# Kernel tuning notes

Measured on AMD Instinct MI355X. Metric: run time of the kernel, lower is better.

The kernel has to match this reference:

```python
import jax, jax.numpy as jnp
import numpy as np

B, N, D, H, A = 1024, 16, 64, 64, 64
TAU = 0.01   # gumbel-softmax temperature from the source
EPS = 1e-10


def setup_inputs() -> dict:
    key = jax.random.key(0)
    ks = jax.random.split(key, 23)

    def rn(k, shape, s=0.05):
        return jax.random.normal(k, shape, dtype=jnp.float32) * s

    return {
        "obs": jax.random.normal(ks[0], (B, N, D), dtype=jnp.float32),
        "hidden_state": jax.random.normal(ks[1], (B * N, A), dtype=jnp.float32),
        "gumbel_u": jax.random.uniform(ks[2], (B * N * (N - 1), 2), dtype=jnp.float32,
                                       minval=1e-6, maxval=1.0 - 1e-6),
        "W_enc": rn(ks[3], (D, H)), "b_enc": rn(ks[4], (H,)),
        "Wih_f": rn(ks[5], (3 * H, 2 * H)), "Whh_f": rn(ks[6], (3 * H, H)),
        "bih_f": rn(ks[7], (3 * H,)), "bhh_f": rn(ks[8], (3 * H,)),
        "Wih_b": rn(ks[9], (3 * H, 2 * H)), "Whh_b": rn(ks[10], (3 * H, H)),
        "bih_b": rn(ks[11], (3 * H,)), "bhh_b": rn(ks[12], (3 * H,)),
        "W_hard": rn(ks[13], (2 * H, 2)), "b_hard": rn(ks[14], (2,)),
        "Wq": rn(ks[15], (H, A)), "Wk": rn(ks[16], (H, A)),
        "Wv": rn(ks[17], (H, A)), "b_v": rn(ks[18], (A,)),
        "Wih_c": rn(ks[19], (3 * A, A)), "Whh_c": rn(ks[20], (3 * A, A)),
        "bih_c": rn(ks[21], (3 * A,)), "bhh_c": rn(ks[22], (3 * A,)),
    }


def _gru_scan(x_seq, Wih, Whh, bih, bhh):
    # x_seq: [T, BN, 2H]; PyTorch GRU gate order r, z, n. Input projection
    # for all timesteps is precomputed (one big GEMM) outside the scan.
    gi = jnp.einsum('tbd,gd->tbg', x_seq, Wih) + bih  # [T, BN, 3H]
    h0 = jnp.zeros((x_seq.shape[1], Whh.shape[1]), x_seq.dtype)

    def step(h, gi_t):
        gh = h @ Whh.T + bhh
        i_r, i_z, i_n = jnp.split(gi_t, 3, axis=-1)
        h_r, h_z, h_n = jnp.split(gh, 3, axis=-1)
        r = jax.nn.sigmoid(i_r + h_r)
        z = jax.nn.sigmoid(i_z + h_z)
        n = jnp.tanh(i_n + r * h_n)
        h_new = (1.0 - z) * n + z * h
        return h_new, h_new

    _, out = jax.lax.scan(step, h0, gi)
    return out  # [T, BN, H]


def _gru_cell(x, h, Wih, Whh, bih, bhh):
    gi = x @ Wih.T + bih
    gh = h @ Whh.T + bhh
    i_r, i_z, i_n = jnp.split(gi, 3, axis=-1)
    h_r, h_z, h_n = jnp.split(gh, 3, axis=-1)
    r = jax.nn.sigmoid(i_r + h_r)
    z = jax.nn.sigmoid(i_z + h_z)
    n = jnp.tanh(i_n + r * h_n)
    return (1.0 - z) * n + z * h


def reference(obs, hidden_state, gumbel_u, W_enc, b_enc,
              Wih_f, Whh_f, bih_f, bhh_f, Wih_b, Whh_b, bih_b, bhh_b,
              W_hard, b_hard, Wq, Wk, Wv, b_v,
              Wih_c, Whh_c, bih_c, bhh_c):
    b, n, d = obs.shape
    h_enc = jax.nn.relu(obs @ W_enc + b_enc)          # [B, N, H]
    h_flat = h_enc.reshape(-1, H)                      # [B*N, H]

    # static neighbor index table: row i lists all j != i
    j_idx = np.array([[j for j in range(n) if j != i] for i in range(n)])  # [N, N-1]

    # pairwise concat features, vectorized (replaces the double python loop)
    h_j = h_enc[:, j_idx]                               # [B, N, N-1, H]
    h_i = jnp.broadcast_to(h_enc[:, :, None, :], h_j.shape)
    pair = jnp.concatenate([h_i, h_j], axis=-1)        # [B, N, N-1, 2H]
    input_hard = pair.transpose(2, 0, 1, 3).reshape(n - 1, b * n, 2 * H)

    # bidirectional GRU over the N-1 neighbor axis
    out_f = _gru_scan(input_hard, Wih_f, Whh_f, bih_f, bhh_f)
    out_b = _gru_scan(input_hard[::-1], Wih_b, Whh_b, bih_b, bhh_b)[::-1]
    h_hard = jnp.concatenate([out_f, out_b], axis=-1)  # [N-1, B*N, 2H]
    h_hard = h_hard.transpose(1, 0, 2).reshape(-1, 2 * H)

    # hard gate: gumbel-softmax (soft sample, tau=0.01), take channel 1
    logits = h_hard @ W_hard + b_hard                   # [B*N*(N-1), 2]
    g = -jnp.log(-jnp.log(gumbel_u + EPS) + EPS)
    hard = jax.nn.softmax((logits + g) / TAU, axis=-1)
    hard_w = hard[:, 1].reshape(b, n, n - 1)            # [B, N, N-1]

    # scaled dot-product attention over neighbors j != i
    q = (h_flat @ Wq).reshape(b, n, A)
    k = (h_flat @ Wk).reshape(b, n, A)
    v = jax.nn.relu(h_flat @ Wv + b_v).reshape(b, n, A)
    k_j = k[:, j_idx]                                   # [B, N, N-1, A]
    v_j = v[:, j_idx]
    score = jnp.einsum('bna,bnja->bnj', q, k_j) / float(np.sqrt(A))
    soft = jax.nn.softmax(score, axis=-1)
    x = jnp.einsum('bnja,bnj->bna', v_j, soft * hard_w).reshape(b * n, A)

    return _gru_cell(x, hidden_state, Wih_c, Whh_c, bih_c, bhh_c)
```

## Files before the change

kernel.cpp:

```cpp
#include <hip/hip_runtime.h>
#include <hip/hip_bf16.h>
#include <stdint.h>

#define NNODE 16384
#define TAU_ 0.01f
#define EPSG 1e-10f

#define OFF_WENC 0
#define OFF_BENC 4096
#define OFF_WIHF_H 4160
#define OFF_WIHF_L 16448
#define OFF_WHHF_H 28736
#define OFF_BIHF 41024
#define OFF_BHHF 41216
#define OFF_WIHB_H 41408
#define OFF_WIHB_L 53696
#define OFF_WHHB_H 65984
#define OFF_BIHB 78272
#define OFF_BHHB 78464
#define OFF_WHARD 78656
#define OFF_BHARD 78912
#define OFF_WQT_H 78914
#define OFF_WQT_L 80962
#define OFF_WKT_H 83010
#define OFF_WKT_L 85058
#define OFF_WVT_H 87106
#define OFF_WVT_L 89154
#define OFF_BV 91202
#define OFF_WIHC_H 91266
#define OFF_WIHC_L 97410
#define OFF_WHHC_H 103554
#define OFF_WHHC_L 109698
#define OFF_BIHC 115842
#define OFF_BHHC 116034
#define OFF_WENCT_H 118784
#define OFF_WENCT_L 120832
#define OFF_YF 131072
#define OFF_YB (OFF_YF + 491520)
#define WS_FLOATS (OFF_YB + 491520)

typedef float  v4f __attribute__((ext_vector_type(4)));
typedef short  v8s __attribute__((ext_vector_type(8)));

__device__ __forceinline__ float rcpf(float x){ return __builtin_amdgcn_rcpf(x); }
__device__ __forceinline__ float sigf(float x){ return rcpf(1.0f + __expf(-x)); }
__device__ __forceinline__ float tanhfast(float x){ return 1.0f - 2.0f*rcpf(__expf(2.0f*x)+1.0f); }
__device__ __forceinline__ unsigned short f2bf(float f){
  __hip_bfloat16 h = __float2bfloat16(f);
  return *reinterpret_cast<unsigned short*>(&h);
}
__device__ __forceinline__ float bf2f(unsigned short u){
  union { unsigned int i; float f; } v; v.i = ((unsigned int)u) << 16; return v.f;
}

struct Prep {
  const float* s[20];
  int n[20];
  int o[20];
};
__global__ void k_prep(Prep p, float* __restrict__ ws){
  int a = blockIdx.y;
  int i = blockIdx.x * blockDim.x + threadIdx.x;
  if (i < p.n[a]) ws[p.o[a] + i] = p.s[a][i];
}

__global__ void k_prep2(const float* __restrict__ wenc,
                        const float* __restrict__ wihf, const float* __restrict__ wihb,
                        const float* __restrict__ whhf, const float* __restrict__ whhb,
                        const float* __restrict__ wq,   const float* __restrict__ wk,
                        const float* __restrict__ wv,   const float* __restrict__ wihc,
                        const float* __restrict__ whhc,
                        float* __restrict__ ws){
  int a = blockIdx.y;
  int i = blockIdx.x * blockDim.x + threadIdx.x;
  if (a == 0 || (a >= 5 && a <= 7)){
    if (i < 4096){
      const float* src = (a==0) ? wenc : (a==5) ? wq : (a==6) ? wk : wv;
      int oh = (a==0) ? OFF_WENCT_H : (a==5) ? OFF_WQT_H : (a==6) ? OFF_WKT_H : OFF_WVT_H;
      int ol = (a==0) ? OFF_WENCT_L : oh + 2048;
      float x = src[((i & 63) << 6) | (i >> 6)];
      unsigned short h = f2bf(x);
      unsigned short l = f2bf(x - bf2f(h));
      ((unsigned short*)(ws + oh))[i] = h;
      ((unsigned short*)(ws + ol))[i] = l;
    }
  } else if (a == 1 || a == 2){
    if (i < 24576){
      float x = (a == 1 ? wihf : wihb)[i];
      unsigned short h = f2bf(x);
      unsigned short l = f2bf(x - bf2f(h));
      ((unsigned short*)(ws + (a == 1 ? OFF_WIHF_H : OFF_WIHB_H)))[i] = h;
      ((unsigned short*)(ws + (a == 1 ? OFF_WIHF_L : OFF_WIHB_L)))[i] = l;
    }
  } else if (a == 3 || a == 4){
    if (i < 12288){
      float x = (a == 3 ? whhf : whhb)[i];
      ((unsigned short*)(ws + (a == 3 ? OFF_WHHF_H : OFF_WHHB_H)))[i] = f2bf(x);
    }
  } else {
    if (i < 12288){
      float x = (a == 8 ? wihc : whhc)[i];
      unsigned short h = f2bf(x);
      unsigned short l = f2bf(x - bf2f(h));
      int oh = (a == 8 ? OFF_WIHC_H : OFF_WHHC_H);
      ((unsigned short*)(ws + oh))[i] = h;
      ((unsigned short*)(ws + oh + 6144))[i] = l;
    }
  }
}

__global__ __launch_bounds__(256, 2) void k_main(const float* __restrict__ obs,
                                                 const float* __restrict__ hid,
                                                 const float* __restrict__ gum,
                                                 float* __restrict__ ws,
                                                 float* __restrict__ out){
  __shared__ float smem[10176];
  float* s_u2 = smem;
  unsigned short* s_B = (unsigned short*)(smem + 6272);
  unsigned short* s_obs_h = s_B;
  unsigned short* s_obs_l = s_B + 1152;
  float* s_red = smem + 9088;
  float* s_y   = smem + 9216;
  float* s_q  = smem;
  float* s_k  = smem + 1088;
  float* s_v  = smem + 2176;
  float* s_co = smem + 3264;

  const int tid = threadIdx.x;
  const int nl  = tid & 63;
  const int grp = __builtin_amdgcn_readfirstlane(tid >> 6);
  const int dir = grp >> 1;
  const int lw  = grp & 1;
  const int hi2 = grp;
  const int q4  = nl >> 4;
  const int i_c = nl & 15;
  const int node = i_c;
  const int base = blockIdx.x * 16;

  {
    float4 a = *(const float4*)&obs[base*64 + tid*4];
    int nn = tid >> 4, d0 = (tid & 15)*4;
    unsigned short hh[4], ll[4];
    float xs[4] = {a.x,a.y,a.z,a.w};
    #pragma unroll
    for (int e = 0; e < 4; e++){
      hh[e] = f2bf(xs[e]);
      ll[e] = f2bf(xs[e] - bf2f(hh[e]));
    }
    *(uint2*)&s_obs_h[nn*72 + d0] = make_uint2((unsigned)hh[0] | ((unsigned)hh[1]<<16),
                                               (unsigned)hh[2] | ((unsigned)hh[3]<<16));
    *(uint2*)&s_obs_l[nn*72 + d0] = make_uint2((unsigned)ll[0] | ((unsigned)ll[1]<<16),
                                               (unsigned)ll[2] | ((unsigned)ll[3]<<16));
  }
  __syncthreads();

  const float* benc = ws + OFF_BENC;
  const unsigned short* wtH = (const unsigned short*)(ws + OFF_WENCT_H);
  const unsigned short* wtL = (const unsigned short*)(ws + OFF_WENCT_L);
  v4f dEnc;
  {
    v8s obH[2], obL[2];
    #pragma unroll
    for (int kc = 0; kc < 2; kc++){
      int ba = node*72 + kc*32 + q4*8;
      obH[kc] = *(const v8s*)&s_obs_h[ba];
      obL[kc] = *(const v8s*)&s_obs_l[ba];
    }
    float4 bi = *(const float4*)&benc[16*hi2 + 4*q4];
    v4f d = (v4f){bi.x, bi.y, bi.z, bi.w};
    #pragma unroll
    for (int kc = 0; kc < 2; kc++){
      int aa = (16*hi2 + i_c)*64 + kc*32 + q4*8;
      v8s aH = *(const v8s*)&wtH[aa];
      v8s aL = *(const v8s*)&wtL[aa];
      d = __builtin_amdgcn_mfma_f32_16x16x32_bf16(aH, obH[kc], d, 0,0,0);
      d = __builtin_amdgcn_mfma_f32_16x16x32_bf16(aH, obL[kc], d, 0,0,0);
      d = __builtin_amdgcn_mfma_f32_16x16x32_bf16(aL, obH[kc], d, 0,0,0);
    }
    dEnc = d;
  }
  __syncthreads();
  {
    unsigned short hh[4], ll[4];
    #pragma unroll
    for (int r = 0; r < 4; r++){
      float v = fmaxf(dEnc[r], 0.0f);
      hh[r] = f2bf(v);
      ll[r] = f2bf(v - bf2f(hh[r]));
    }
    int wa = node*72 + 16*hi2 + 4*q4;
    *(uint2*)&s_obs_h[wa] = make_uint2((unsigned)hh[0] | ((unsigned)hh[1]<<16),
                                       (unsigned)hh[2] | ((unsigned)hh[3]<<16));
    *(uint2*)&s_obs_l[wa] = make_uint2((unsigned)ll[0] | ((unsigned)ll[1]<<16),
                                       (unsigned)ll[2] | ((unsigned)ll[3]<<16));
  }
  __syncthreads();

  v8s hbH[2], hbL[2];
  #pragma unroll
  for (int kc = 0; kc < 2; kc++){
    int ba = node*72 + kc*32 + q4*8;
    hbH[kc] = *(const v8s*)&s_obs_h[ba];
    hbL[kc] = *(const v8s*)&s_obs_l[ba];
  }

  v4f dq, dk, dv;
  {
    const unsigned short* wqH = (const unsigned short*)(ws + OFF_WQT_H);
    const unsigned short* wqL = (const unsigned short*)(ws + OFF_WQT_L);
    const unsigned short* wkH = (const unsigned short*)(ws + OFF_WKT_H);
    const unsigned short* wkL = (const unsigned short*)(ws + OFF_WKT_L);
    const unsigned short* wvH = (const unsigned short*)(ws + OFF_WVT_H);
    const unsigned short* wvL = (const unsigned short*)(ws + OFF_WVT_L);
    const float* bv = ws + OFF_BV;
    v4f q_ = (v4f){0.f,0.f,0.f,0.f};
    v4f k_ = (v4f){0.f,0.f,0.f,0.f};
    float4 b4 = *(const float4*)&bv[16*hi2 + 4*q4];
    v4f v_ = (v4f){b4.x, b4.y, b4.z, b4.w};
    #pragma unroll
    for (int kc = 0; kc < 2; kc++){
      int ai = (16*hi2 + i_c)*64 + kc*32 + q4*8;
      v8s aH = *(const v8s*)&wqH[ai]; v8s aL = *(const v8s*)&wqL[ai];
      q_ = __builtin_amdgcn_mfma_f32_16x16x32_bf16(aH, hbH[kc], q_, 0,0,0);
      q_ = __builtin_amdgcn_mfma_f32_16x16x32_bf16(aH, hbL[kc], q_, 0,0,0);
      q_ = __builtin_amdgcn_mfma_f32_16x16x32_bf16(aL, hbH[kc], q_, 0,0,0);
      aH = *(const v8s*)&wkH[ai]; aL = *(const v8s*)&wkL[ai];
      k_ = __builtin_amdgcn_mfma_f32_16x16x32_bf16(aH, hbH[kc], k_, 0,0,0);
      k_ = __builtin_amdgcn_mfma_f32_16x16x32_bf16(aH, hbL[kc], k_, 0,0,0);
      k_ = __builtin_amdgcn_mfma_f32_16x16x32_bf16(aL, hbH[kc], k_, 0,0,0);
      aH = *(const v8s*)&wvH[ai]; aL = *(const v8s*)&wvL[ai];
      v_ = __builtin_amdgcn_mfma_f32_16x16x32_bf16(aH, hbH[kc], v_, 0,0,0);
      v_ = __builtin_amdgcn_mfma_f32_16x16x32_bf16(aH, hbL[kc], v_, 0,0,0);
      v_ = __builtin_amdgcn_mfma_f32_16x16x32_bf16(aL, hbH[kc], v_, 0,0,0);
    }
    dq = q_; dk = k_; dv = v_;
  }

  const float* bih = ws + (dir ? OFF_BIHB : OFF_BIHF);
  const float* bhh = ws + (dir ? OFF_BHHB : OFF_BHHF);
  const unsigned short* wiH = (const unsigned short*)(ws + (dir ? OFF_WIHB_H : OFF_WIHF_H));
  const unsigned short* wiL = (const unsigned short*)(ws + (dir ? OFF_WIHB_L : OFF_WIHF_L));
  const unsigned short* whH = (const unsigned short*)(ws + (dir ? OFF_WHHB_H : OFF_WHHF_H));
  float* myu2 = s_u2 + dir*3136;

  #pragma unroll
  for (int m = 0; m < 6; m++){
    int T = 6*lw + m;
    v4f d = (v4f){0.f,0.f,0.f,0.f};
    #pragma unroll
    for (int kc = 0; kc < 2; kc++){
      int aa = (16*T + i_c)*128 + 64 + kc*32 + q4*8;
      v8s aH = *(const v8s*)&wiH[aa];
      v8s aL = *(const v8s*)&wiL[aa];
      d = __builtin_amdgcn_mfma_f32_16x16x32_bf16(aH, hbH[kc], d, 0,0,0);
      d = __builtin_amdgcn_mfma_f32_16x16x32_bf16(aH, hbL[kc], d, 0,0,0);
      d = __builtin_amdgcn_mfma_f32_16x16x32_bf16(aL, hbH[kc], d, 0,0,0);
    }
    *(v4f*)&myu2[node*196 + 16*T + 4*q4] = d;
  }

  v4f cbr[2], cbz[2], cbn[2], bhn4[2];
  #pragma unroll
  for (int g = 0; g < 3; g++){
    #pragma unroll
    for (int t2 = 0; t2 < 2; t2++){
      int row0 = 64*g + 32*lw + 16*t2 + 4*q4;
      float4 bi = *(const float4*)&bih[row0];
      v4f d;
      if (g < 2){
        float4 bh = *(const float4*)&bhh[row0];
        d = (v4f){bi.x+bh.x, bi.y+bh.y, bi.z+bh.z, bi.w+bh.w};
      } else {
        d = (v4f){bi.x, bi.y, bi.z, bi.w};
      }
      int T = (64*g + 32*lw + 16*t2) >> 4;
      #pragma unroll
      for (int kc = 0; kc < 2; kc++){
        int aa = (16*T + i_c)*128 + kc*32 + q4*8;
        v8s aH = *(const v8s*)&wiH[aa];
        v8s aL = *(const v8s*)&wiL[aa];
        d = __builtin_amdgcn_mfma_f32_16x16x32_bf16(aH, hbH[kc], d, 0,0,0);
        d = __builtin_amdgcn_mfma_f32_16x16x32_bf16(aH, hbL[kc], d, 0,0,0);
        d = __builtin_amdgcn_mfma_f32_16x16x32_bf16(aL, hbH[kc], d, 0,0,0);
      }
      if (g == 0) cbr[t2] = d; else if (g == 1) cbz[t2] = d; else cbn[t2] = d;
    }
  }
  #pragma unroll
  for (int t2 = 0; t2 < 2; t2++){
    int row0 = 128 + 32*lw + 16*t2 + 4*q4;
    float4 nh = *(const float4*)&bhh[row0];
    bhn4[t2] = (v4f){nh.x, nh.y, nh.z, nh.w};
  }

  v8s afr[2][2], afz[2][2], afn[2][2];
  #pragma unroll
  for (int t2 = 0; t2 < 2; t2++){
    #pragma unroll
    for (int kc = 0; kc < 2; kc++){
      #pragma unroll
      for (int g = 0; g < 3; g++){
        int row = g*64 + 32*lw + 16*t2 + i_c;
        v8s a = *(const v8s*)&whH[row*64 + kc*32 + q4*8];
        if (g == 0) afr[t2][kc] = a; else if (g == 1) afz[t2][kc] = a; else afn[t2][kc] = a;
      }
    }
  }

  const float* whard = ws + OFF_WHARD + dir*128;
  float wh0[8], wh1[8];
  #pragma unroll
  for (int t2 = 0; t2 < 2; t2++){
    #pragma unroll
    for (int r = 0; r < 4; r++){
      int l = 32*lw + 16*t2 + 4*q4 + r;
      wh0[t2*4+r] = whard[l*2];
      wh1[t2*4+r] = whard[l*2+1];
    }
  }
  __syncthreads();

  unsigned short* myh = s_B + dir*2816;
  float hv[8];
  #pragma unroll
  for (int m = 0; m < 8; m++) hv[m] = 0.0f;

  for (int kk = 0; kk < 15; kk++){
    const int t  = dir ? (14 - kk) : kk;
    const int j  = t + (t >= i_c ? 1 : 0);
    const int jl = j;
    const int rb = kk & 1;
    const int wb = (kk + 1) & 1;

    v8s b0, b1;
    if (kk > 0){
      const unsigned short* rp = myh + rb*1408 + node*88 + q4*8;
      b0 = *(const v8s*)(rp);
      b1 = *(const v8s*)(rp + 32);
    }

    float a0p = 0.f, a1p = 0.f;
    #pragma unroll
    for (int t2 = 0; t2 < 2; t2++){
      int l0 = 32*lw + 16*t2 + 4*q4;
      v4f dr = cbr[t2], dz = cbz[t2];
      v4f dn = (v4f){0.f,0.f,0.f,0.f};
      if (kk > 0){
        dr = __builtin_amdgcn_mfma_f32_16x16x32_bf16(afr[t2][0], b0, dr, 0,0,0);
        dr = __builtin_amdgcn_mfma_f32_16x16x32_bf16(afr[t2][1], b1, dr, 0,0,0);
        dz = __builtin_amdgcn_mfma_f32_16x16x32_bf16(afz[t2][0], b0, dz, 0,0,0);
        dz = __builtin_amdgcn_mfma_f32_16x16x32_bf16(afz[t2][1], b1, dz, 0,0,0);
        dn = __builtin_amdgcn_mfma_f32_16x16x32_bf16(afn[t2][0], b0, dn, 0,0,0);
        dn = __builtin_amdgcn_mfma_f32_16x16x32_bf16(afn[t2][1], b1, dn, 0,0,0);
      }
      v4f ur = *(const v4f*)&myu2[jl*196 +       l0];
      v4f uz = *(const v4f*)&myu2[jl*196 +  64 + l0];
      v4f un = *(const v4f*)&myu2[jl*196 + 128 + l0];
      float hn[4];
      #pragma unroll
      for (int r = 0; r < 4; r++){
        float rg = sigf(dr[r] + ur[r]);
        float zg = sigf(dz[r] + uz[r]);
        float ng = tanhfast(cbn[t2][r] + un[r] + rg*(bhn4[t2][r] + dn[r]));
        float hnew = (1.0f - zg)*ng + zg*hv[t2*4+r];
        hv[t2*4+r] = hnew;
        hn[r] = hnew;
        a0p += hnew*wh0[t2*4+r];
        a1p += hnew*wh1[t2*4+r];
      }
      unsigned int p0 = (unsigned int)f2bf(hn[0]) | ((unsigned int)f2bf(hn[1]) << 16);
      unsigned int p1 = (unsigned int)f2bf(hn[2]) | ((unsigned int)f2bf(hn[3]) << 16);
      *(uint2*)(myh + wb*1408 + node*88 + l0) = make_uint2(p0, p1);
    }

    a0p += __shfl_xor(a0p, 16); a0p += __shfl_xor(a0p, 32);
    a1p += __shfl_xor(a1p, 16); a1p += __shfl_xor(a1p, 32);
    float* sr = s_red + dir*64 + rb*32;
    if (lw == 0 && q4 == 0)
      *(float2*)&sr[node*2] = make_float2(a0p, a1p);
    __syncthreads();
    if (lw == 1 && q4 == 0){
      float2 pp = *(const float2*)&sr[node*2];
      *(float2*)&s_y[dir*480 + (node*15 + t)*2] = make_float2(a0p + pp.x, a1p + pp.y);
    }
  }
  __syncthreads();

  {
    *(v4f*)&s_q[node*68 + 16*hi2 + 4*q4] = dq;
    #pragma unroll
    for (int r = 0; r < 4; r++){
      s_k[(16*hi2 + 4*q4 + r)*17 + node] = dk[r];
      s_v[(16*hi2 + 4*q4 + r)*17 + node] = fmaxf(dv[r], 0.f);
    }
  }
  __syncthreads();

  const int n2  = tid >> 3;
  const int asl = tid & 7;
  if (tid < 128){
    float4 aq0 = *(const float4*)&s_q[n2*68 + asl*8];
    float4 aq1 = *(const float4*)&s_q[n2*68 + asl*8 + 4];
    float sc[15];
    #pragma unroll
    for (int t = 0; t < 15; t++){
      int jl = t + (t >= n2 ? 1 : 0);
      const float* kp = s_k + (asl*8)*17 + jl;
      float s = aq0.x*kp[0]  + aq0.y*kp[17]  + aq0.z*kp[34]  + aq0.w*kp[51]
              + aq1.x*kp[68] + aq1.y*kp[85]  + aq1.z*kp[102] + aq1.w*kp[119];
      s += __shfl_xor(s, 1); s += __shfl_xor(s, 2); s += __shfl_xor(s, 4);
      sc[t] = s * 0.125f;
    }
    float m = sc[0];
    #pragma unroll
    for (int t = 1; t < 15; t++) m = fmaxf(m, sc[t]);
    float den = 0.f;
    #pragma unroll
    for (int t = 0; t < 15; t++) den += __expf(sc[t]-m);
    float rden = rcpf(den);
    const float bh0 = ws[OFF_BHARD], bh1 = ws[OFF_BHARD+1];
    #pragma unroll
    for (int t = 0; t < 15; t++){
      if ((t & 7) == asl){
        int yi = (n2*15 + t)*2;
        float y0 = s_y[yi]     + s_y[480 + yi]     + bh0;
        float y1 = s_y[yi + 1] + s_y[480 + yi + 1] + bh1;
        float2 u2 = *(const float2*)&gum[((base + n2)*15 + t)*2];
        float g0 = -__logf(-__logf(u2.x + EPSG) + EPSG);
        float g1 = -__logf(-__logf(u2.y + EPSG) + EPSG);
        float w  = sigf(((y1+g1) - (y0+g0)) * (1.0f/TAU_));
        s_co[t*16 + n2] = __expf(sc[t]-m)*rden*w;
      }
    }
  }
  __syncthreads();

  unsigned short* s_xh  = s_B;
  unsigned short* s_xl  = s_B + 1152;
  unsigned short* s_h0h = s_B + 2304;
  unsigned short* s_h0l = s_B + 3456;
  if (tid < 128){
    float xa[8];
    #pragma unroll
    for (int il = 0; il < 8; il++) xa[il] = 0.f;
    #pragma unroll
    for (int t = 0; t < 15; t++){
      float c = s_co[t*16 + n2];
      int jl = t + (t >= n2 ? 1 : 0);
      const float* vp = s_v + (asl*8)*17 + jl;
      xa[0] += c*vp[0];   xa[1] += c*vp[17];  xa[2] += c*vp[34];  xa[3] += c*vp[51];
      xa[4] += c*vp[68];  xa[5] += c*vp[85];  xa[6] += c*vp[102]; xa[7] += c*vp[119];
    }
    union { v8s v; unsigned short u[8]; } XH, XL;
    #pragma unroll
    for (int e = 0; e < 8; e++){
      XH.u[e] = f2bf(xa[e]);
      XL.u[e] = f2bf(xa[e] - bf2f(XH.u[e]));
    }
    *(v8s*)&s_xh[n2*72 + asl*8] = XH.v;
    *(v8s*)&s_xl[n2*72 + asl*8] = XL.v;
  }
  {
    float4 a = *(const float4*)&hid[base*64 + tid*4];
    int nn = tid >> 4, d0 = (tid & 15)*4;
    unsigned short hh[4], ll[4];
    float xs[4] = {a.x,a.y,a.z,a.w};
    #pragma unroll
    for (int e = 0; e < 4; e++){
      hh[e] = f2bf(xs[e]);
      ll[e] = f2bf(xs[e] - bf2f(hh[e]));
    }
    *(uint2*)&s_h0h[nn*72 + d0] = make_uint2((unsigned)hh[0] | ((unsigned)hh[1]<<16),
                                             (unsigned)hh[2] | ((unsigned)hh[3]<<16));
    *(uint2*)&s_h0l[nn*72 + d0] = make_uint2((unsigned)ll[0] | ((unsigned)ll[1]<<16),
                                             (unsigned)ll[2] | ((unsigned)ll[3]<<16));
  }
  __syncthreads();

  {
    v8s xbH[2], xbL[2], h0H[2], h0L[2];
    #pragma unroll
    for (int kc = 0; kc < 2; kc++){
      int ba = node*72 + kc*32 + q4*8;
      xbH[kc] = *(const v8s*)&s_xh[ba];  xbL[kc] = *(const v8s*)&s_xl[ba];
      h0H[kc] = *(const v8s*)&s_h0h[ba]; h0L[kc] = *(const v8s*)&s_h0l[ba];
    }
    const unsigned short* wiH2 = (const unsigned short*)(ws + OFF_WIHC_H);
    const unsigned short* wiL2 = (const unsigned short*)(ws + OFF_WIHC_L);
    const unsigned short* whH2 = (const unsigned short*)(ws + OFF_WHHC_H);
    const unsigned short* whL2 = (const unsigned short*)(ws + OFF_WHHC_L);
    const float* bihc = ws + OFF_BIHC; const float* bhhc = ws + OFF_BHHC;
    v4f gi[3], gh[3];
    #pragma unroll
    for (int g = 0; g < 3; g++){
      int row0 = g*64 + 16*hi2 + 4*q4;
      float4 bi = *(const float4*)&bihc[row0];
      float4 bh = *(const float4*)&bhhc[row0];
      v4f di, dh;
      if (g < 2){
        di = (v4f){bi.x+bh.x, bi.y+bh.y, bi.z+bh.z, bi.w+bh.w};
        dh = (v4f){0.f,0.f,0.f,0.f};
      } else {
        di = (v4f){bi.x, bi.y, bi.z, bi.w};
        dh = (v4f){bh.x, bh.y, bh.z, bh.w};
      }
      #pragma unroll
      for (int kc = 0; kc < 2; kc++){
        int ai = (g*64 + 16*hi2 + i_c)*64 + kc*32 + q4*8;
        v8s aH = *(const v8s*)&wiH2[ai]; v8s aL = *(const v8s*)&wiL2[ai];
        di = __builtin_amdgcn_mfma_f32_16x16x32_bf16(aH, xbH[kc], di, 0,0,0);
        di = __builtin_amdgcn_mfma_f32_16x16x32_bf16(aH, xbL[kc], di, 0,0,0);
        di = __builtin_amdgcn_mfma_f32_16x16x32_bf16(aL, xbH[kc], di, 0,0,0);
        aH = *(const v8s*)&whH2[ai]; aL = *(const v8s*)&whL2[ai];
        dh = __builtin_amdgcn_mfma_f32_16x16x32_bf16(aH, h0H[kc], dh, 0,0,0);
        dh = __builtin_amdgcn_mfma_f32_16x16x32_bf16(aH, h0L[kc], dh, 0,0,0);
        dh = __builtin_amdgcn_mfma_f32_16x16x32_bf16(aL, h0H[kc], dh, 0,0,0);
      }
      gi[g] = di; gh[g] = dh;
    }
    int l0 = 16*hi2 + 4*q4;
    float4 h04 = *(const float4*)&hid[(base+node)*64 + l0];
    float hh4[4] = {h04.x, h04.y, h04.z, h04.w};
    float ho[4];
    #pragma unroll
    for (int r = 0; r < 4; r++){
      float rg = sigf(gi[0][r] + gh[0][r]);
      float zg = sigf(gi[1][r] + gh[1][r]);
      float ng = tanhfast(gi[2][r] + rg*gh[2][r]);
      ho[r] = (1.0f - zg)*ng + zg*hh4[r];
    }
    *(float4*)&out[(base+node)*64 + l0] = make_float4(ho[0], ho[1], ho[2], ho[3]);
  }
}

extern "C" void kernel_launch(void* const* d_in, const int* in_sizes, int n_in,
                              void* d_out, int out_size, void* d_ws, size_t ws_size,
                              hipStream_t stream){
  if (ws_size < (size_t)WS_FLOATS * sizeof(float)) return;
  float* ws = (float*)d_ws;
  static const int offs[20] = {OFF_WENC, OFF_BENC, 0, 0, OFF_BIHF, OFF_BHHF,
      0, 0, OFF_BIHB, OFF_BHHB, OFF_WHARD, OFF_BHARD, 0, 0, 0,
      OFF_BV, 0, 0, OFF_BIHC, OFF_BHHC};
  Prep p;
  for (int i = 0; i < 20; i++){
    p.s[i] = (const float*)d_in[3 + i];
    p.n[i] = in_sizes[3 + i];
    p.o[i] = offs[i];
  }
  p.n[2] = 0; p.n[3] = 0; p.n[6] = 0; p.n[7] = 0;
  p.n[12] = 0; p.n[13] = 0; p.n[14] = 0;
  p.n[16] = 0; p.n[17] = 0;
  hipLaunchKernelGGL(k_prep, dim3(96, 20), dim3(256), 0, stream, p, ws);
  hipLaunchKernelGGL(k_prep2, dim3(96, 10), dim3(256), 0, stream,
                     (const float*)d_in[3], (const float*)d_in[5], (const float*)d_in[9],
                     (const float*)d_in[6], (const float*)d_in[10],
                     (const float*)d_in[15], (const float*)d_in[16], (const float*)d_in[17],
                     (const float*)d_in[19], (const float*)d_in[20], ws);
  hipLaunchKernelGGL(k_main, dim3(1024), dim3(256), 0, stream,
                     (const float*)d_in[0], (const float*)d_in[1],
                     (const float*)d_in[2], ws, (float*)d_out);
}
```

Baseline: 192.4 us.

## Merge prep kernels, prefetch GRU input gates, widen attention to all threads

Folds the two weight-prep kernels into one launch with a 30-row grid, removing one kernel launch. In the bidirectional GRU loop, the per-step input-gate values are loaded from shared memory one step ahead into registers, so the loads overlap the barrier rather than sitting on the critical path. The attention score and value-aggregation phases now use all 256 threads with 4 elements per lane instead of 128 threads with 8, which adds one shuffle stage but halves per-thread work. Register pressure rises from the prefetch buffers.

Result: faster. 188.4 us (median of 2 runs) (-2.1%).

```diff
diff --git a/kernel.cpp b/kernel.cpp
--- a/kernel.cpp
+++ b/kernel.cpp
@@ -58,21 +58,21 @@
   int n[20];
   int o[20];
 };
-__global__ void k_prep(Prep p, float* __restrict__ ws){
+__global__ void k_prep(Prep p,
+                       const float* __restrict__ wenc,
+                       const float* __restrict__ wihf, const float* __restrict__ wihb,
+                       const float* __restrict__ whhf, const float* __restrict__ whhb,
+                       const float* __restrict__ wq,   const float* __restrict__ wk,
+                       const float* __restrict__ wv,   const float* __restrict__ wihc,
+                       const float* __restrict__ whhc,
+                       float* __restrict__ ws){
   int a = blockIdx.y;
   int i = blockIdx.x * blockDim.x + threadIdx.x;
-  if (i < p.n[a]) ws[p.o[a] + i] = p.s[a][i];
-}
-
-__global__ void k_prep2(const float* __restrict__ wenc,
-                        const float* __restrict__ wihf, const float* __restrict__ wihb,
-                        const float* __restrict__ whhf, const float* __restrict__ whhb,
-                        const float* __restrict__ wq,   const float* __restrict__ wk,
-                        const float* __restrict__ wv,   const float* __restrict__ wihc,
-                        const float* __restrict__ whhc,
-                        float* __restrict__ ws){
-  int a = blockIdx.y;
-  int i = blockIdx.x * blockDim.x + threadIdx.x;
+  if (a < 20){
+    if (i < p.n[a]) ws[p.o[a] + i] = p.s[a][i];
+    return;
+  }
+  a -= 20;
   if (a == 0 || (a >= 5 && a <= 7)){
     if (i < 4096){
       const float* src = (a==0) ? wenc : (a==5) ? wq : (a==6) ? wk : wv;
@@ -325,10 +325,24 @@
   #pragma unroll
   for (int m = 0; m < 8; m++) hv[m] = 0.0f;
 
+  #define JL_OF(kk2) ({ int t_ = dir ? (14 - (kk2)) : (kk2);                  \
+                        int j_ = t_ + (t_ >= i_c ? 1 : 0);                     \
+                        j_ < 0 ? 0 : (j_ > 15 ? 15 : j_); })
+
+  v4f uP[2][3];
+  {
+    int jl0 = JL_OF(0);
+    #pragma unroll
+    for (int t2 = 0; t2 < 2; t2++){
+      int l0 = 32*lw + 16*t2 + 4*q4;
+      uP[t2][0] = *(const v4f*)&myu2[jl0*196 +       l0];
+      uP[t2][1] = *(const v4f*)&myu2[jl0*196 +  64 + l0];
+      uP[t2][2] = *(const v4f*)&myu2[jl0*196 + 128 + l0];
+    }
+  }
+
   for (int kk = 0; kk < 15; kk++){
     const int t  = dir ? (14 - kk) : kk;
-    const int j  = t + (t >= i_c ? 1 : 0);
-    const int jl = j;
     const int rb = kk & 1;
     const int wb = (kk + 1) & 1;
 
@@ -353,15 +367,12 @@
         dn = __builtin_amdgcn_mfma_f32_16x16x32_bf16(afn[t2][0], b0, dn, 0,0,0);
         dn = __builtin_amdgcn_mfma_f32_16x16x32_bf16(afn[t2][1], b1, dn, 0,0,0);
       }
-      v4f ur = *(const v4f*)&myu2[jl*196 +       l0];
-      v4f uz = *(const v4f*)&myu2[jl*196 +  64 + l0];
-      v4f un = *(const v4f*)&myu2[jl*196 + 128 + l0];
       float hn[4];
       #pragma unroll
       for (int r = 0; r < 4; r++){
-        float rg = sigf(dr[r] + ur[r]);
-        float zg = sigf(dz[r] + uz[r]);
-        float ng = tanhfast(cbn[t2][r] + un[r] + rg*(bhn4[t2][r] + dn[r]));
+        float rg = sigf(dr[r] + uP[t2][0][r]);
+        float zg = sigf(dz[r] + uP[t2][1][r]);
+        float ng = tanhfast(cbn[t2][r] + uP[t2][2][r] + rg*(bhn4[t2][r] + dn[r]));
         float hnew = (1.0f - zg)*ng + zg*hv[t2*4+r];
         hv[t2*4+r] = hnew;
         hn[r] = hnew;
@@ -378,12 +389,24 @@
     float* sr = s_red + dir*64 + rb*32;
     if (lw == 0 && q4 == 0)
       *(float2*)&sr[node*2] = make_float2(a0p, a1p);
+
+    {
+      int jlN = JL_OF(kk + 1);
+      #pragma unroll
+      for (int t2 = 0; t2 < 2; t2++){
+        int l0 = 32*lw + 16*t2 + 4*q4;
+        uP[t2][0] = *(const v4f*)&myu2[jlN*196 +       l0];
+        uP[t2][1] = *(const v4f*)&myu2[jlN*196 +  64 + l0];
+        uP[t2][2] = *(const v4f*)&myu2[jlN*196 + 128 + l0];
+      }
+    }
     __syncthreads();
     if (lw == 1 && q4 == 0){
       float2 pp = *(const float2*)&sr[node*2];
       *(float2*)&s_y[dir*480 + (node*15 + t)*2] = make_float2(a0p + pp.x, a1p + pp.y);
     }
   }
+  #undef JL_OF
   __syncthreads();
 
   {
@@ -396,19 +419,18 @@
   }
   __syncthreads();
 
-  const int n2  = tid >> 3;
-  const int asl = tid & 7;
-  if (tid < 128){
-    float4 aq0 = *(const float4*)&s_q[n2*68 + asl*8];
-    float4 aq1 = *(const float4*)&s_q[n2*68 + asl*8 + 4];
+  const int n2  = tid >> 4;
+  const int asl = tid & 15;
+  {
+    float4 aq0 = *(const float4*)&s_q[n2*68 + asl*4];
     float sc[15];
     #pragma unroll
     for (int t = 0; t < 15; t++){
       int jl = t + (t >= n2 ? 1 : 0);
-      const float* kp = s_k + (asl*8)*17 + jl;
-      float s = aq0.x*kp[0]  + aq0.y*kp[17]  + aq0.z*kp[34]  + aq0.w*kp[51]
-              + aq1.x*kp[68] + aq1.y*kp[85]  + aq1.z*kp[102] + aq1.w*kp[119];
-      s += __shfl_xor(s, 1); s += __shfl_xor(s, 2); s += __shfl_xor(s, 4);
+      const float* kp = s_k + (asl*4)*17 + jl;
+      float s = aq0.x*kp[0] + aq0.y*kp[17] + aq0.z*kp[34] + aq0.w*kp[51];
+      s += __shfl_xor(s, 1); s += __shfl_xor(s, 2);
+      s += __shfl_xor(s, 4); s += __shfl_xor(s, 8);
       sc[t] = s * 0.125f;
     }
     float m = sc[0];
@@ -421,7 +443,7 @@
     const float bh0 = ws[OFF_BHARD], bh1 = ws[OFF_BHARD+1];
     #pragma unroll
     for (int t = 0; t < 15; t++){
-      if ((t & 7) == asl){
+      if ((t & 15) == asl){
         int yi = (n2*15 + t)*2;
         float y0 = s_y[yi]     + s_y[480 + yi]     + bh0;
         float y1 = s_y[yi + 1] + s_y[480 + yi + 1] + bh1;
@@ -439,26 +461,27 @@
   unsigned short* s_xl  = s_B + 1152;
   unsigned short* s_h0h = s_B + 2304;
   unsigned short* s_h0l = s_B + 3456;
-  if (tid < 128){
-    float xa[8];
-    #pragma unroll
-    for (int il = 0; il < 8; il++) xa[il] = 0.f;
+  {
+    float xa[4];
+    #pragma unroll
+    for (int il = 0; il < 4; il++) xa[il] = 0.f;
     #pragma unroll
     for (int t = 0; t < 15; t++){
       float c = s_co[t*16 + n2];
       int jl = t + (t >= n2 ? 1 : 0);
-      const float* vp = s_v + (asl*8)*17 + jl;
-      xa[0] += c*vp[0];   xa[1] += c*vp[17];  xa[2] += c*vp[34];  xa[3] += c*vp[51];
-      xa[4] += c*vp[68];  xa[5] += c*vp[85];  xa[6] += c*vp[102]; xa[7] += c*vp[119];
-    }
-    union { v8s v; unsigned short u[8]; } XH, XL;
-    #pragma unroll
-    for (int e = 0; e < 8; e++){
-      XH.u[e] = f2bf(xa[e]);
-      XL.u[e] = f2bf(xa[e] - bf2f(XH.u[e]));
-    }
-    *(v8s*)&s_xh[n2*72 + asl*8] = XH.v;
-    *(v8s*)&s_xl[n2*72 + asl*8] = XL.v;
+      const float* vp = s_v + (asl*4)*17 + jl;
+      xa[0] += c*vp[0]; xa[1] += c*vp[17]; xa[2] += c*vp[34]; xa[3] += c*vp[51];
+    }
+    unsigned short xh[4], xl[4];
+    #pragma unroll
+    for (int e = 0; e < 4; e++){
+      xh[e] = f2bf(xa[e]);
+      xl[e] = f2bf(xa[e] - bf2f(xh[e]));
+    }
+    *(uint2*)&s_xh[n2*72 + asl*4] = make_uint2((unsigned)xh[0] | ((unsigned)xh[1]<<16),
+                                               (unsigned)xh[2] | ((unsigned)xh[3]<<16));
+    *(uint2*)&s_xl[n2*72 + asl*4] = make_uint2((unsigned)xl[0] | ((unsigned)xl[1]<<16),
+                                               (unsigned)xl[2] | ((unsigned)xl[3]<<16));
   }
   {
     float4 a = *(const float4*)&hid[base*64 + tid*4];
@@ -550,8 +573,7 @@
   p.n[2] = 0; p.n[3] = 0; p.n[6] = 0; p.n[7] = 0;
   p.n[12] = 0; p.n[13] = 0; p.n[14] = 0;
   p.n[16] = 0; p.n[17] = 0;
-  hipLaunchKernelGGL(k_prep, dim3(96, 20), dim3(256), 0, stream, p, ws);
-  hipLaunchKernelGGL(k_prep2, dim3(96, 10), dim3(256), 0, stream,
+  hipLaunchKernelGGL(k_prep, dim3(96, 30), dim3(256), 0, stream, p,
                      (const float*)d_in[3], (const float*)d_in[5], (const float*)d_in[9],
                      (const float*)d_in[6], (const float*)d_in[10],
                      (const float*)d_in[15], (const float*)d_in[16], (const float*)d_in[17],
```
